# Kernel optimization log

Hardware: AMD Instinct MI355X
Metric: run time of the kernel (lower is better)

Reference implementation:

```python
import jax, jax.numpy as jnp
import numpy as np

D_MODEL = 1024
NUM_HEADS = 16
DEPTH = D_MODEL // NUM_HEADS


def setup_inputs() -> dict:
    key = jax.random.key(0)
    ks = jax.random.split(key, 6)
    B, S = 2, 2048
    scale = 1.0 / np.sqrt(D_MODEL)
    return {
        "q": jax.random.normal(ks[0], (B, S, D_MODEL), jnp.float32),
        "k": jax.random.normal(ks[1], (B, S, D_MODEL), jnp.float32),
        "v": jax.random.normal(ks[2], (B, S, D_MODEL), jnp.float32),
        "wq": jax.random.normal(ks[3], (D_MODEL, D_MODEL), jnp.float32) * scale,
        "wk": jax.random.normal(ks[4], (D_MODEL, D_MODEL), jnp.float32) * scale,
        "wv": jax.random.normal(ks[5], (D_MODEL, D_MODEL), jnp.float32) * scale,
    }


def reference(q, k, v, wq, wk, wv):
    B, S, _ = q.shape
    # Linear projections (nn.Linear: x @ W.T), then split heads -> [B,H,S,depth]
    def split(x):
        return x.reshape(B, -1, NUM_HEADS, DEPTH).transpose(0, 2, 1, 3)
    Q = split(q @ wq.T)
    K = split(k @ wk.T)
    V = split(v @ wv.T)
    scores = jnp.einsum("bhqd,bhkd->bhqk", Q, K) / np.sqrt(DEPTH).astype(np.float32)
    attn = jax.nn.softmax(scores, axis=-1)
    out = jnp.einsum("bhqk,bhkd->bhqd", attn, V)
    # merge heads; note: original forward never applies self.dense
    return out.transpose(0, 2, 1, 3).reshape(B, S, D_MODEL)
```

## Files before the change

### kernel.cpp

```cpp
#include <hip/hip_runtime.h>
#include <hip/hip_bf16.h>
#include <stdint.h>

#define B_SZ 2
#define S_LEN 2048
#define DM 1024
#define NH 16
#define DEPTH 64
#define M_ROWS (B_SZ * S_LEN)
#define SCALE_Q 0.1803368801111144f

typedef __attribute__((ext_vector_type(8))) short bf16x8;
typedef __attribute__((ext_vector_type(4))) float f32x4;
typedef __attribute__((ext_vector_type(16))) float f32x16;

__device__ __forceinline__ unsigned short f2bf(float x) {
    union { float f; unsigned u; } a; a.f = x;
    unsigned r = a.u + 0x7FFF + ((a.u >> 16) & 1);
    return (unsigned short)(r >> 16);
}

__device__ __forceinline__ void async_ld16(const unsigned short* g, void* l) {
    __builtin_amdgcn_global_load_lds(
        (const __attribute__((address_space(1))) void*)g,
        (__attribute__((address_space(3))) void*)l,
        16, 0, 0);
}


__global__ __launch_bounds__(256)
void convert_kernel(const float* __restrict__ q, const float* __restrict__ k,
                    const float* __restrict__ v, const float* __restrict__ wq,
                    const float* __restrict__ wk, const float* __restrict__ wv,
                    unsigned short* __restrict__ dst) {
    const int z = blockIdx.y;
    const float* src = (z == 0) ? q : (z == 1) ? k : (z == 2) ? v
                     : (z == 3) ? wq : (z == 4) ? wk : wv;
    const size_t n4  = (z < 3) ? ((size_t)M_ROWS * DM / 4) : ((size_t)DM * DM / 4);
    const size_t off = (z < 3) ? ((size_t)z * M_ROWS * DM)
                               : ((size_t)3 * M_ROWS * DM + (size_t)(z - 3) * DM * DM);
    unsigned short* d = dst + off;
    const size_t stride = (size_t)gridDim.x * blockDim.x;
    for (size_t i = (size_t)blockIdx.x * blockDim.x + threadIdx.x; i < n4; i += stride) {
        float4 x = ((const float4*)src)[i];
        ushort4 p;
        p.x = f2bf(x.x); p.y = f2bf(x.y); p.z = f2bf(x.z); p.w = f2bf(x.w);
        ((ushort4*)d)[i] = p;
    }
}

__global__ __launch_bounds__(256)
void proj_gemm3_kernel(const unsigned short* __restrict__ Xall,
                       const unsigned short* __restrict__ Wall,
                       unsigned short* __restrict__ Call) {
    __shared__ unsigned short As[128 * 64];
    __shared__ unsigned short Bs[128 * 64];

    const int z = blockIdx.z;
    const unsigned short* X = Xall + (size_t)z * M_ROWS * DM;
    const unsigned short* W = Wall + (size_t)z * DM * DM;
    unsigned short* C = Call + (size_t)z * M_ROWS * DM;

    const int tid  = threadIdx.x;
    const int wave = tid >> 6;
    const int lane = tid & 63;
    const int l32  = lane & 31;
    const int s    = lane >> 5;
    const int m0 = blockIdx.x * 128;
    const int n0 = blockIdx.y * 128;
    const int wm = (wave >> 1) * 64;
    const int wn = (wave & 1) * 64;

    const int r8 = lane >> 3;
    const int sc = (lane & 7) ^ r8;

    f32x16 acc[2][2];
#pragma unroll
    for (int mi = 0; mi < 2; ++mi)
#pragma unroll
        for (int ni = 0; ni < 2; ++ni)
#pragma unroll
            for (int r = 0; r < 16; ++r) acc[mi][ni][r] = 0.f;

    for (int k0 = 0; k0 < DM; k0 += 64) {
#pragma unroll
        for (int i = 0; i < 4; ++i) {
            const int r = i * 32 + wave * 8 + r8;
            async_ld16(X + (size_t)(m0 + r) * DM + k0 + sc * 8,
                       (char*)As + i * 4096 + wave * 1024);
            async_ld16(W + (size_t)(n0 + r) * DM + k0 + sc * 8,
                       (char*)Bs + i * 4096 + wave * 1024);
        }
        __syncthreads();

#pragma unroll
        for (int ch = 0; ch < 4; ++ch) {
            bf16x8 af[2], bfr[2];
#pragma unroll
            for (int mi = 0; mi < 2; ++mi) {
                const int row = wm + mi * 32 + l32;
                af[mi] = *(const bf16x8*)&As[row * 64 + (((2 * ch + s) ^ (row & 7)) * 8)];
            }
#pragma unroll
            for (int ni = 0; ni < 2; ++ni) {
                const int row = wn + ni * 32 + l32;
                bfr[ni] = *(const bf16x8*)&Bs[row * 64 + (((2 * ch + s) ^ (row & 7)) * 8)];
            }
#pragma unroll
            for (int mi = 0; mi < 2; ++mi)
#pragma unroll
                for (int ni = 0; ni < 2; ++ni)
                    acc[mi][ni] = __builtin_amdgcn_mfma_f32_32x32x16_bf16(
                        af[mi], bfr[ni], acc[mi][ni], 0, 0, 0);
        }
        __syncthreads();
    }

    const float scale = (z == 0) ? SCALE_Q : 1.0f;
#pragma unroll
    for (int mi = 0; mi < 2; ++mi)
#pragma unroll
        for (int ni = 0; ni < 2; ++ni)
#pragma unroll
            for (int r = 0; r < 16; ++r) {
                const int row = m0 + wm + mi * 32 + (r & 3) + 8 * (r >> 2) + 4 * s;
                const int col = n0 + wn + ni * 32 + l32;
                C[(size_t)row * DM + col] = f2bf(acc[mi][ni][r] * scale);
            }
}

__global__ __launch_bounds__(256)
void vtrans_kernel(const unsigned short* __restrict__ Vp,
                   unsigned short* __restrict__ Vt) {
    __shared__ unsigned short Ls[64 * 72];
    const int tr = blockIdx.x;
    const int h  = blockIdx.y;
    const int tid = threadIdx.x;

#pragma unroll
    for (int i = 0; i < 2; ++i) {
        const int id = i * 256 + tid;
        const int r = id >> 3, c = id & 7;
        bf16x8 v8 = *(const bf16x8*)&Vp[(size_t)(tr * 64 + r) * DM + h * 64 + c * 8];
        *(bf16x8*)&Ls[r * 72 + ((c ^ (r & 7)) * 8)] = v8;
    }
    __syncthreads();

    const int b = tr >> 5;
    const int col0 = (tr & 31) * 64;
#pragma unroll
    for (int i = 0; i < 2; ++i) {
        const int id = i * 256 + tid;
        const int d = id >> 3, c2 = id & 7;
        unsigned short tmp[8];
#pragma unroll
        for (int j = 0; j < 8; ++j) {
            const int t = c2 * 8 + j;
            tmp[j] = Ls[t * 72 + (((d >> 3) ^ (t & 7)) * 8) + (d & 7)];
        }
        *(bf16x8*)&Vt[(size_t)((b * NH + h) * DEPTH + d) * S_LEN + col0 + c2 * 8] =
            *(const bf16x8*)tmp;
    }
}

__global__ __launch_bounds__(64)
void attn4_kernel(const unsigned short* __restrict__ Qp,
                  const unsigned short* __restrict__ Kp,
                  const unsigned short* __restrict__ Vt,
                  float* __restrict__ out) {
    __shared__ __align__(16) char smem[40960];
    unsigned short* Ks = (unsigned short*)smem;
    unsigned short* Vs = (unsigned short*)(smem + 16384);
    unsigned short* Ps = (unsigned short*)(smem + 32768);

    const int lane = threadIdx.x & 63;
    const int l32  = lane & 31;
    const int s    = lane >> 5;
    const int q0 = blockIdx.x * 64;
    const int h  = blockIdx.y;
    const int b  = blockIdx.z;

    const int r8 = lane >> 3;
    const int sc = (lane & 7) ^ r8;

    const unsigned short* Kg = Kp + (size_t)(b * S_LEN) * DM + h * DEPTH;
    const unsigned short* Vg = Vt + (size_t)((b * NH + h) * DEPTH) * S_LEN;

    bf16x8 qf[2][4];
#pragma unroll
    for (int nq = 0; nq < 2; ++nq) {
        const unsigned short* p =
            Qp + (size_t)(b * S_LEN + q0 + nq * 32 + l32) * DM + h * DEPTH;
#pragma unroll
        for (int ch = 0; ch < 4; ++ch)
            qf[nq][ch] = *(const bf16x8*)(p + ch * 16 + s * 8);
    }

    f32x16 oacc[2][2];
    float lacc[2] = {0.f, 0.f};
#pragma unroll
    for (int db = 0; db < 2; ++db)
#pragma unroll
        for (int nq = 0; nq < 2; ++nq)
#pragma unroll
            for (int r = 0; r < 16; ++r) oacc[db][nq][r] = 0.f;

#pragma unroll
    for (int i = 0; i < 8; ++i) {
        async_ld16(Kg + (size_t)(i * 8 + r8) * DM + sc * 8, (char*)Ks + i * 1024);
        async_ld16(Vg + (size_t)(i * 8 + r8) * S_LEN + sc * 8, (char*)Vs + i * 1024);
    }

    for (int it = 0; it < S_LEN / 64; ++it) {
        const int buf = it & 1;
        if (it < S_LEN / 64 - 1) {
            const int t1 = (it + 1) * 64;
            char* kd = (char*)Ks + (buf ^ 1) * 8192;
            char* vd = (char*)Vs + (buf ^ 1) * 8192;
#pragma unroll
            for (int i = 0; i < 8; ++i) {
                async_ld16(Kg + (size_t)(t1 + i * 8 + r8) * DM + sc * 8,
                           kd + i * 1024);
                async_ld16(Vg + (size_t)(i * 8 + r8) * S_LEN + t1 + sc * 8,
                           vd + i * 1024);
            }
            __builtin_amdgcn_s_waitcnt(0x4F70);
        } else {
            __builtin_amdgcn_s_waitcnt(0x0F70);
        }
        __builtin_amdgcn_sched_barrier(0);

        const unsigned short* Kb = Ks + buf * 4096;
        const unsigned short* Vb = Vs + buf * 4096;

#pragma unroll
        for (int tb = 0; tb < 2; ++tb) {
            f32x16 s0, s1;
#pragma unroll
            for (int r = 0; r < 16; ++r) { s0[r] = 0.f; s1[r] = 0.f; }
            const int trow = tb * 32 + l32;
#pragma unroll
            for (int ch = 0; ch < 4; ++ch) {
                bf16x8 kf = *(const bf16x8*)
                    &Kb[trow * 64 + (((2 * ch + s) ^ (trow & 7)) * 8)];
                s0 = __builtin_amdgcn_mfma_f32_32x32x16_bf16(kf, qf[0][ch], s0, 0, 0, 0);
                s1 = __builtin_amdgcn_mfma_f32_32x32x16_bf16(kf, qf[1][ch], s1, 0, 0, 0);
            }
#pragma unroll
            for (int nq = 0; nq < 2; ++nq) {
                const int qq = nq * 32 + l32;
#pragma unroll
                for (int a = 0; a < 4; ++a) {
                    union { float f; unsigned u; } e0, e1, e2, e3;
                    e0.f = __builtin_amdgcn_exp2f(nq ? s1[4 * a + 0] : s0[4 * a + 0]);
                    e1.f = __builtin_amdgcn_exp2f(nq ? s1[4 * a + 1] : s0[4 * a + 1]);
                    e2.f = __builtin_amdgcn_exp2f(nq ? s1[4 * a + 2] : s0[4 * a + 2]);
                    e3.f = __builtin_amdgcn_exp2f(nq ? s1[4 * a + 3] : s0[4 * a + 3]);
                    union { unsigned u; float f; } t0, t1, t2, t3;
                    t0.u = e0.u & 0xFFFF0000u; t1.u = e1.u & 0xFFFF0000u;
                    t2.u = e2.u & 0xFFFF0000u; t3.u = e3.u & 0xFFFF0000u;
                    lacc[nq] += (t0.f + t1.f) + (t2.f + t3.f);
                    const int slot = (4 * tb + a) ^ (qq & 7);
                    *(unsigned*)&Ps[qq * 64 + slot * 8 + 4 * s] =
                        (e0.u >> 16) | (e1.u & 0xFFFF0000u);
                    *(unsigned*)&Ps[qq * 64 + slot * 8 + 4 * s + 2] =
                        (e2.u >> 16) | (e3.u & 0xFFFF0000u);
                }
            }
        }
        __builtin_amdgcn_sched_barrier(0);

#pragma unroll
        for (int ch = 0; ch < 4; ++ch) {
            bf16x8 pf0 = *(const bf16x8*)
                &Ps[l32 * 64 + (((2 * ch + s) ^ (l32 & 7)) * 8)];
            bf16x8 pf1 = *(const bf16x8*)
                &Ps[(32 + l32) * 64 + (((2 * ch + s) ^ (l32 & 7)) * 8)];
#pragma unroll
            for (int db = 0; db < 2; ++db) {
                const int drow = db * 32 + l32;
                bf16x8 vf = *(const bf16x8*)
                    &Vb[drow * 64 + (((2 * ch + s) ^ (drow & 7)) * 8)];
                oacc[db][0] = __builtin_amdgcn_mfma_f32_32x32x16_bf16(
                    vf, pf0, oacc[db][0], 0, 0, 0);
                oacc[db][1] = __builtin_amdgcn_mfma_f32_32x32x16_bf16(
                    vf, pf1, oacc[db][1], 0, 0, 0);
            }
        }
        __builtin_amdgcn_sched_barrier(0);
    }

    const float l0 = lacc[0] + __shfl_xor(lacc[0], 32, 64);
    const float l1 = lacc[1] + __shfl_xor(lacc[1], 32, 64);
    const float inv0 = 1.0f / l0, inv1 = 1.0f / l1;

    __builtin_amdgcn_s_waitcnt(0xC07F);
    __builtin_amdgcn_sched_barrier(0);
    float* Of = (float*)(smem + 16384);
#pragma unroll
    for (int db = 0; db < 2; ++db)
#pragma unroll
        for (int nq = 0; nq < 2; ++nq) {
            const int qq = nq * 32 + l32;
            const float inv = nq ? inv1 : inv0;
#pragma unroll
            for (int r = 0; r < 16; ++r) {
                const int d = db * 32 + (r & 3) + 8 * (r >> 2) + 4 * s;
                Of[qq * 68 + d] = oacc[db][nq][r] * inv;
            }
        }
    __builtin_amdgcn_sched_barrier(0);
#pragma unroll
    for (int i = 0; i < 16; ++i) {
        const int row = i * 4 + (lane >> 4);
        const int c4 = lane & 15;
        float4 v = *(const float4*)&Of[row * 68 + c4 * 4];
        *(float4*)&out[(size_t)(b * S_LEN + q0 + row) * DM + h * DEPTH + c4 * 4] = v;
    }
}

#define LDK 72

__global__ __launch_bounds__(256)
void proj_gemm_kernel(const float* __restrict__ q, const float* __restrict__ k,
                      const float* __restrict__ v, const float* __restrict__ wq,
                      const float* __restrict__ wk, const float* __restrict__ wv,
                      unsigned short* __restrict__ Qp, unsigned short* __restrict__ Kp,
                      unsigned short* __restrict__ Vp) {
    __shared__ unsigned short As[128 * LDK];
    __shared__ unsigned short Bs[128 * LDK];

    const int z = blockIdx.z;
    const float* __restrict__ X = (z == 0) ? q : (z == 1) ? k : v;
    const float* __restrict__ W = (z == 0) ? wq : (z == 1) ? wk : wv;
    unsigned short* __restrict__ C = (z == 0) ? Qp : (z == 1) ? Kp : Vp;

    const int tid  = threadIdx.x;
    const int wave = tid >> 6;
    const int lane = tid & 63;
    const int quad = lane >> 4;
    const int l16  = lane & 15;
    const int m0 = blockIdx.x * 128;
    const int n0 = blockIdx.y * 128;
    const int wm = (wave >> 1) * 64;
    const int wn = (wave & 1) * 64;

    f32x4 acc[4][4];
#pragma unroll
    for (int mt = 0; mt < 4; ++mt)
#pragma unroll
        for (int nt = 0; nt < 4; ++nt)
            acc[mt][nt] = (f32x4){0.f, 0.f, 0.f, 0.f};

    for (int k0 = 0; k0 < DM; k0 += 64) {
#pragma unroll
        for (int vv = 0; vv < 8; ++vv) {
            int vecid = tid + 256 * vv;
            int r  = vecid >> 4;
            int c4 = vecid & 15;
            const float4 xa = *(const float4*)&X[(size_t)(m0 + r) * DM + k0 + c4 * 4];
            ushort4 pa;
            pa.x = f2bf(xa.x); pa.y = f2bf(xa.y); pa.z = f2bf(xa.z); pa.w = f2bf(xa.w);
            *(ushort4*)&As[r * LDK + c4 * 4] = pa;
            const float4 xb = *(const float4*)&W[(size_t)(n0 + r) * DM + k0 + c4 * 4];
            ushort4 pb;
            pb.x = f2bf(xb.x); pb.y = f2bf(xb.y); pb.z = f2bf(xb.z); pb.w = f2bf(xb.w);
            *(ushort4*)&Bs[r * LDK + c4 * 4] = pb;
        }
        __syncthreads();

#pragma unroll
        for (int kc = 0; kc < 2; ++kc) {
            bf16x8 af[4], bfr[4];
#pragma unroll
            for (int mt = 0; mt < 4; ++mt)
                af[mt] = *(const bf16x8*)&As[(wm + mt * 16 + l16) * LDK + kc * 32 + quad * 8];
#pragma unroll
            for (int nt = 0; nt < 4; ++nt)
                bfr[nt] = *(const bf16x8*)&Bs[(wn + nt * 16 + l16) * LDK + kc * 32 + quad * 8];
#pragma unroll
            for (int mt = 0; mt < 4; ++mt)
#pragma unroll
                for (int nt = 0; nt < 4; ++nt)
                    acc[mt][nt] = __builtin_amdgcn_mfma_f32_16x16x32_bf16(
                        af[mt], bfr[nt], acc[mt][nt], 0, 0, 0);
        }
        __syncthreads();
    }

#pragma unroll
    for (int mt = 0; mt < 4; ++mt)
#pragma unroll
        for (int nt = 0; nt < 4; ++nt)
#pragma unroll
            for (int r = 0; r < 4; ++r) {
                int row = m0 + wm + mt * 16 + quad * 4 + r;
                int col = n0 + wn + nt * 16 + l16;
                C[(size_t)row * DM + col] = f2bf(acc[mt][nt][r]);
            }
}

__global__ __launch_bounds__(256)
void attn_kernel(const unsigned short* __restrict__ Qp,
                 const unsigned short* __restrict__ Kp,
                 const unsigned short* __restrict__ Vp,
                 float* __restrict__ out) {
    __shared__ unsigned short Ks[64 * LDK];
    __shared__ unsigned short Vtl[64 * LDK];
    __shared__ unsigned short Ps[4 * 16 * LDK];

    const int tid  = threadIdx.x;
    const int wave = tid >> 6;
    const int lane = tid & 63;
    const int quad = lane >> 4;
    const int l16  = lane & 15;
    const int q0 = blockIdx.x * 64;
    const int h  = blockIdx.y;
    const int b  = blockIdx.z;
    const int wbase = wave * 16 * LDK;

    bf16x8 qf[2];
    {
        size_t row = (size_t)b * S_LEN + q0 + wave * 16 + l16;
        const unsigned short* p = Qp + row * DM + h * DEPTH;
        qf[0] = *(const bf16x8*)(p + quad * 8);
        qf[1] = *(const bf16x8*)(p + 32 + quad * 8);
    }

    float m_i[4], l_i[4];
    f32x4 accO[4];
#pragma unroll
    for (int r = 0; r < 4; ++r) { m_i[r] = -1e30f; l_i[r] = 0.f; }
#pragma unroll
    for (int f = 0; f < 4; ++f) accO[f] = (f32x4){0.f, 0.f, 0.f, 0.f};

    for (int t0 = 0; t0 < S_LEN; t0 += 64) {
#pragma unroll
        for (int vv = 0; vv < 2; ++vv) {
            int vecid = tid + 256 * vv;
            int r  = vecid >> 3;
            int cv = vecid & 7;
            size_t grow = (size_t)(b * S_LEN + t0 + r) * DM + h * DEPTH + cv * 8;
            *(bf16x8*)&Ks[r * LDK + cv * 8] = *(const bf16x8*)(Kp + grow);
            bf16x8 vvv = *(const bf16x8*)(Vp + grow);
#pragma unroll
            for (int j = 0; j < 8; ++j)
                Vtl[(cv * 8 + j) * LDK + r] = ((const unsigned short*)&vvv)[j];
        }
        __syncthreads();

        f32x4 sc4[4];
#pragma unroll
        for (int nt = 0; nt < 4; ++nt) {
            f32x4 a = (f32x4){0.f, 0.f, 0.f, 0.f};
            bf16x8 kf0 = *(const bf16x8*)&Ks[(nt * 16 + l16) * LDK + quad * 8];
            bf16x8 kf1 = *(const bf16x8*)&Ks[(nt * 16 + l16) * LDK + 32 + quad * 8];
            a = __builtin_amdgcn_mfma_f32_16x16x32_bf16(qf[0], kf0, a, 0, 0, 0);
            a = __builtin_amdgcn_mfma_f32_16x16x32_bf16(qf[1], kf1, a, 0, 0, 0);
            sc4[nt] = a;
        }
#pragma unroll
        for (int nt = 0; nt < 4; ++nt)
#pragma unroll
            for (int r = 0; r < 4; ++r) sc4[nt][r] *= 0.125f;

#pragma unroll
        for (int r = 0; r < 4; ++r) {
            float mx = fmaxf(fmaxf(sc4[0][r], sc4[1][r]), fmaxf(sc4[2][r], sc4[3][r]));
#pragma unroll
            for (int off = 1; off < 16; off <<= 1)
                mx = fmaxf(mx, __shfl_xor(mx, off, 64));
            float mnew = fmaxf(m_i[r], mx);
            float alpha = __expf(m_i[r] - mnew);
            float rs = 0.f;
#pragma unroll
            for (int nt = 0; nt < 4; ++nt) {
                float p = __expf(sc4[nt][r] - mnew);
                sc4[nt][r] = p;
                rs += p;
            }
#pragma unroll
            for (int off = 1; off < 16; off <<= 1)
                rs += __shfl_xor(rs, off, 64);
            l_i[r] = l_i[r] * alpha + rs;
            m_i[r] = mnew;
#pragma unroll
            for (int f = 0; f < 4; ++f) accO[f][r] *= alpha;
        }

#pragma unroll
        for (int nt = 0; nt < 4; ++nt)
#pragma unroll
            for (int r = 0; r < 4; ++r)
                Ps[wbase + (quad * 4 + r) * LDK + nt * 16 + l16] = f2bf(sc4[nt][r]);
        __syncthreads();

        bf16x8 pf0 = *(const bf16x8*)&Ps[wbase + l16 * LDK + quad * 8];
        bf16x8 pf1 = *(const bf16x8*)&Ps[wbase + l16 * LDK + 32 + quad * 8];
#pragma unroll
        for (int f = 0; f < 4; ++f) {
            bf16x8 vf0 = *(const bf16x8*)&Vtl[(f * 16 + l16) * LDK + quad * 8];
            bf16x8 vf1 = *(const bf16x8*)&Vtl[(f * 16 + l16) * LDK + 32 + quad * 8];
            accO[f] = __builtin_amdgcn_mfma_f32_16x16x32_bf16(pf0, vf0, accO[f], 0, 0, 0);
            accO[f] = __builtin_amdgcn_mfma_f32_16x16x32_bf16(pf1, vf1, accO[f], 0, 0, 0);
        }
        __syncthreads();
    }

#pragma unroll
    for (int f = 0; f < 4; ++f)
#pragma unroll
        for (int r = 0; r < 4; ++r) {
            size_t row = (size_t)b * S_LEN + q0 + wave * 16 + quad * 4 + r;
            out[row * DM + h * DEPTH + f * 16 + l16] = accO[f][r] / l_i[r];
        }
}

extern "C" void kernel_launch(void* const* d_in, const int* in_sizes, int n_in,
                              void* d_out, int out_size, void* d_ws, size_t ws_size,
                              hipStream_t stream) {
    const float* q  = (const float*)d_in[0];
    const float* k  = (const float*)d_in[1];
    const float* v  = (const float*)d_in[2];
    const float* wq = (const float*)d_in[3];
    const float* wk = (const float*)d_in[4];
    const float* wv = (const float*)d_in[5];
    float* out = (float*)d_out;

    unsigned short* ws = (unsigned short*)d_ws;
    const size_t NPROJ = (size_t)M_ROWS * DM;
    const size_t NW    = (size_t)DM * DM;

    const size_t need = (3 * NPROJ + 3 * NW + 3 * NPROJ) * sizeof(unsigned short);

    if (ws_size >= need) {
        unsigned short* Xbf = ws;
        unsigned short* Wbf = ws + 3 * NPROJ;
        unsigned short* Cp  = ws + 3 * NPROJ + 3 * NW;
        unsigned short* Qp  = Cp;
        unsigned short* Kp  = Cp + NPROJ;
        unsigned short* Vp  = Cp + 2 * NPROJ;
        unsigned short* Vt  = ws;

        convert_kernel<<<dim3(256, 6), 256, 0, stream>>>(q, k, v, wq, wk, wv, Xbf);
        proj_gemm3_kernel<<<dim3(M_ROWS / 128, DM / 128, 3), 256, 0, stream>>>(Xbf, Wbf, Cp);
        vtrans_kernel<<<dim3(M_ROWS / 64, NH), 256, 0, stream>>>(Vp, Vt);
        attn4_kernel<<<dim3(S_LEN / 64, NH, B_SZ), 64, 0, stream>>>(Qp, Kp, Vt, out);
    } else {
        unsigned short* Qp = ws;
        unsigned short* Kp = ws + NPROJ;
        unsigned short* Vp = ws + 2 * NPROJ;
        proj_gemm_kernel<<<dim3(M_ROWS / 128, DM / 128, 3), 256, 0, stream>>>(
            q, k, v, wq, wk, wv, Qp, Kp, Vp);
        attn_kernel<<<dim3(S_LEN / 64, NH, B_SZ), 256, 0, stream>>>(Qp, Kp, Vp, out);
    }
}
```

Measured before the change: 213.5 us.

## Split attention over key halves with two-wave blocks and a combine pass

Replaces the one-wave attention kernel with two-wave blocks that share K/V tiles in LDS and split the key sequence into two halves across the grid. Each half writes unnormalized partial outputs and row sums, and a new combine kernel adds them and normalizes. K is now staged in 32-row tiles and V in 64-column tiles, with a block barrier each iteration. The aim is more parallelism and better reuse of K/V loads across waves. The cost is extra global traffic for the partial outputs, an extra kernel launch, and per-iteration synchronization.

```diff
diff --git a/kernel.cpp b/kernel.cpp
--- a/kernel.cpp
+++ b/kernel.cpp
@@ -18,6 +18,10 @@
     union { float f; unsigned u; } a; a.f = x;
     unsigned r = a.u + 0x7FFF + ((a.u >> 16) & 1);
     return (unsigned short)(r >> 16);
+}
+
+__device__ __forceinline__ bf16x8 u4_to_bf8(uint4 u) {
+    union { uint4 a; bf16x8 b; } c; c.a = u; return c.b;
 }
 
 __device__ __forceinline__ void async_ld16(const unsigned short* g, void* l) {
@@ -163,28 +167,38 @@
     }
 }
 
-__global__ __launch_bounds__(64)
-void attn4_kernel(const unsigned short* __restrict__ Qp,
+__global__ __launch_bounds__(128, 2)
+void attn8_kernel(const unsigned short* __restrict__ Qp,
                   const unsigned short* __restrict__ Kp,
                   const unsigned short* __restrict__ Vt,
-                  float* __restrict__ out) {
-    __shared__ __align__(16) char smem[40960];
+                  float* __restrict__ out,
+                  float* __restrict__ Op1,
+                  float* __restrict__ lp) {
+    __shared__ __align__(16) char smem[34816];
     unsigned short* Ks = (unsigned short*)smem;
-    unsigned short* Vs = (unsigned short*)(smem + 16384);
-    unsigned short* Ps = (unsigned short*)(smem + 32768);
-
-    const int lane = threadIdx.x & 63;
+    unsigned short* Vs = (unsigned short*)(smem + 8192);
+    unsigned int*   Ps = (unsigned int*)(smem + 24576);
+
+    const int tid  = threadIdx.x;
+    const int w    = tid >> 6;
+    const int lane = tid & 63;
     const int l32  = lane & 31;
     const int s    = lane >> 5;
-    const int q0 = blockIdx.x * 64;
+    const int r8   = lane >> 3;
+    const int sc   = (lane & 7) ^ r8;
+
+    const int q0 = blockIdx.x * 128 + w * 64;
     const int h  = blockIdx.y;
-    const int b  = blockIdx.z;
-
-    const int r8 = lane >> 3;
-    const int sc = (lane & 7) ^ r8;
-
-    const unsigned short* Kg = Kp + (size_t)(b * S_LEN) * DM + h * DEPTH;
-    const unsigned short* Vg = Vt + (size_t)((b * NH + h) * DEPTH) * S_LEN;
+    const int z  = blockIdx.z;
+    const int b     = z >> 1;
+    const int split = z & 1;
+    const int tbase = split * 1024;
+
+    const unsigned short* Kg = Kp + (size_t)(b * S_LEN + tbase) * DM + h * DEPTH;
+    const unsigned short* Vg = Vt + (size_t)((b * NH + h) * DEPTH) * S_LEN + tbase;
+    float* obase = split ? Op1 : out;
+    float* lbase = lp + (size_t)split * M_ROWS * NH;
+    unsigned int* PsW = Ps + w * 1280;
 
     bf16x8 qf[2][4];
 #pragma unroll
@@ -206,117 +220,155 @@
             for (int r = 0; r < 16; ++r) oacc[db][nq][r] = 0.f;
 
 #pragma unroll
-    for (int i = 0; i < 8; ++i) {
-        async_ld16(Kg + (size_t)(i * 8 + r8) * DM + sc * 8, (char*)Ks + i * 1024);
-        async_ld16(Vg + (size_t)(i * 8 + r8) * S_LEN + sc * 8, (char*)Vs + i * 1024);
-    }
-
-    for (int it = 0; it < S_LEN / 64; ++it) {
-        const int buf = it & 1;
-        if (it < S_LEN / 64 - 1) {
-            const int t1 = (it + 1) * 64;
-            char* kd = (char*)Ks + (buf ^ 1) * 8192;
-            char* vd = (char*)Vs + (buf ^ 1) * 8192;
-#pragma unroll
-            for (int i = 0; i < 8; ++i) {
-                async_ld16(Kg + (size_t)(t1 + i * 8 + r8) * DM + sc * 8,
+    for (int i = 0; i < 2; ++i)
+        async_ld16(Kg + (size_t)(w * 16 + i * 8 + r8) * DM + sc * 8,
+                   (char*)Ks + w * 2048 + i * 1024);
+#pragma unroll
+    for (int i = 0; i < 4; ++i)
+        async_ld16(Vg + (size_t)(w * 32 + i * 8 + r8) * S_LEN + sc * 8,
+                   (char*)Vs + w * 4096 + i * 1024);
+
+    for (int it = 0; it < 32; ++it) {
+        const int kb = it & 1;
+        const int vb = (it >> 1) & 1;
+
+        __syncthreads();
+
+        if (it < 31) {
+            const int tk = (it + 1) * 32;
+            char* kd = (char*)Ks + (kb ^ 1) * 4096 + w * 2048;
+#pragma unroll
+            for (int i = 0; i < 2; ++i)
+                async_ld16(Kg + (size_t)(tk + w * 16 + i * 8 + r8) * DM + sc * 8,
                            kd + i * 1024);
-                async_ld16(Vg + (size_t)(i * 8 + r8) * S_LEN + t1 + sc * 8,
+        }
+        if (!(it & 1) && it < 30) {
+            const int tv = ((it >> 1) + 1) * 64;
+            char* vd = (char*)Vs + (vb ^ 1) * 8192 + w * 4096;
+#pragma unroll
+            for (int i = 0; i < 4; ++i)
+                async_ld16(Vg + (size_t)(w * 32 + i * 8 + r8) * S_LEN + tv + sc * 8,
                            vd + i * 1024);
-            }
-            __builtin_amdgcn_s_waitcnt(0x4F70);
-        } else {
-            __builtin_amdgcn_s_waitcnt(0x0F70);
-        }
-        __builtin_amdgcn_sched_barrier(0);
-
-        const unsigned short* Kb = Ks + buf * 4096;
-        const unsigned short* Vb = Vs + buf * 4096;
-
-#pragma unroll
-        for (int tb = 0; tb < 2; ++tb) {
-            f32x16 s0, s1;
-#pragma unroll
-            for (int r = 0; r < 16; ++r) { s0[r] = 0.f; s1[r] = 0.f; }
-            const int trow = tb * 32 + l32;
-#pragma unroll
-            for (int ch = 0; ch < 4; ++ch) {
-                bf16x8 kf = *(const bf16x8*)
-                    &Kb[trow * 64 + (((2 * ch + s) ^ (trow & 7)) * 8)];
-                s0 = __builtin_amdgcn_mfma_f32_32x32x16_bf16(kf, qf[0][ch], s0, 0, 0, 0);
-                s1 = __builtin_amdgcn_mfma_f32_32x32x16_bf16(kf, qf[1][ch], s1, 0, 0, 0);
-            }
+        }
+
+        const unsigned short* Kb = Ks + kb * 2048;
+        const unsigned short* Vb = Vs + vb * 4096;
+        const int vcb = (it & 1) * 4;
+
+        f32x16 s0, s1;
+#pragma unroll
+        for (int r = 0; r < 16; ++r) { s0[r] = 0.f; s1[r] = 0.f; }
+#pragma unroll
+        for (int ch = 0; ch < 4; ++ch) {
+            bf16x8 kf = *(const bf16x8*)
+                &Kb[l32 * 64 + (((2 * ch + s) ^ (l32 & 7)) * 8)];
+            s0 = __builtin_amdgcn_mfma_f32_32x32x16_bf16(kf, qf[0][ch], s0, 0, 0, 0);
+            s1 = __builtin_amdgcn_mfma_f32_32x32x16_bf16(kf, qf[1][ch], s1, 0, 0, 0);
+        }
+
+#pragma unroll
+        for (int nq = 0; nq < 2; ++nq) {
+            const int qq = nq * 32 + l32;
+            const int xq = (qq ^ (qq >> 2)) & 3;
+#pragma unroll
+            for (int a = 0; a < 4; ++a) {
+                union { float f; unsigned u; } e0, e1, e2, e3;
+                e0.f = __builtin_amdgcn_exp2f(nq ? s1[4 * a + 0] : s0[4 * a + 0]);
+                e1.f = __builtin_amdgcn_exp2f(nq ? s1[4 * a + 1] : s0[4 * a + 1]);
+                e2.f = __builtin_amdgcn_exp2f(nq ? s1[4 * a + 2] : s0[4 * a + 2]);
+                e3.f = __builtin_amdgcn_exp2f(nq ? s1[4 * a + 3] : s0[4 * a + 3]);
+                union { unsigned u; float f; } t0, t1, t2, t3;
+                t0.u = e0.u & 0xFFFF0000u; t1.u = e1.u & 0xFFFF0000u;
+                t2.u = e2.u & 0xFFFF0000u; t3.u = e3.u & 0xFFFF0000u;
+                lacc[nq] += (t0.f + t1.f) + (t2.f + t3.f);
+                uint2 pk;
+                pk.x = (e0.u >> 16) | (e1.u & 0xFFFF0000u);
+                pk.y = (e2.u >> 16) | (e3.u & 0xFFFF0000u);
+                *(uint2*)&PsW[qq * 20 + ((a ^ xq) * 4) + 2 * s] = pk;
+            }
+        }
+
+        asm volatile("" ::: "memory");
+
+#pragma unroll
+        for (int ch = 0; ch < 2; ++ch) {
+            bf16x8 pf[2];
 #pragma unroll
             for (int nq = 0; nq < 2; ++nq) {
                 const int qq = nq * 32 + l32;
-#pragma unroll
-                for (int a = 0; a < 4; ++a) {
-                    union { float f; unsigned u; } e0, e1, e2, e3;
-                    e0.f = __builtin_amdgcn_exp2f(nq ? s1[4 * a + 0] : s0[4 * a + 0]);
-                    e1.f = __builtin_amdgcn_exp2f(nq ? s1[4 * a + 1] : s0[4 * a + 1]);
-                    e2.f = __builtin_amdgcn_exp2f(nq ? s1[4 * a + 2] : s0[4 * a + 2]);
-                    e3.f = __builtin_amdgcn_exp2f(nq ? s1[4 * a + 3] : s0[4 * a + 3]);
-                    union { unsigned u; float f; } t0, t1, t2, t3;
-                    t0.u = e0.u & 0xFFFF0000u; t1.u = e1.u & 0xFFFF0000u;
-                    t2.u = e2.u & 0xFFFF0000u; t3.u = e3.u & 0xFFFF0000u;
-                    lacc[nq] += (t0.f + t1.f) + (t2.f + t3.f);
-                    const int slot = (4 * tb + a) ^ (qq & 7);
-                    *(unsigned*)&Ps[qq * 64 + slot * 8 + 4 * s] =
-                        (e0.u >> 16) | (e1.u & 0xFFFF0000u);
-                    *(unsigned*)&Ps[qq * 64 + slot * 8 + 4 * s + 2] =
-                        (e2.u >> 16) | (e3.u & 0xFFFF0000u);
-                }
-            }
-        }
-        __builtin_amdgcn_sched_barrier(0);
-
-#pragma unroll
-        for (int ch = 0; ch < 4; ++ch) {
-            bf16x8 pf0 = *(const bf16x8*)
-                &Ps[l32 * 64 + (((2 * ch + s) ^ (l32 & 7)) * 8)];
-            bf16x8 pf1 = *(const bf16x8*)
-                &Ps[(32 + l32) * 64 + (((2 * ch + s) ^ (l32 & 7)) * 8)];
+                const int slot = (2 * ch + s) ^ ((qq ^ (qq >> 2)) & 3);
+                uint4 pu = *(const uint4*)&PsW[qq * 20 + slot * 4];
+                pf[nq] = u4_to_bf8(pu);
+            }
 #pragma unroll
             for (int db = 0; db < 2; ++db) {
                 const int drow = db * 32 + l32;
                 bf16x8 vf = *(const bf16x8*)
-                    &Vb[drow * 64 + (((2 * ch + s) ^ (drow & 7)) * 8)];
+                    &Vb[drow * 64 + (((vcb + 2 * ch + s) ^ (drow & 7)) * 8)];
                 oacc[db][0] = __builtin_amdgcn_mfma_f32_32x32x16_bf16(
-                    vf, pf0, oacc[db][0], 0, 0, 0);
+                    vf, pf[0], oacc[db][0], 0, 0, 0);
                 oacc[db][1] = __builtin_amdgcn_mfma_f32_32x32x16_bf16(
-                    vf, pf1, oacc[db][1], 0, 0, 0);
-            }
-        }
-        __builtin_amdgcn_sched_barrier(0);
+                    vf, pf[1], oacc[db][1], 0, 0, 0);
+            }
+        }
+        asm volatile("" ::: "memory");
     }
 
     const float l0 = lacc[0] + __shfl_xor(lacc[0], 32, 64);
     const float l1 = lacc[1] + __shfl_xor(lacc[1], 32, 64);
-    const float inv0 = 1.0f / l0, inv1 = 1.0f / l1;
-
-    __builtin_amdgcn_s_waitcnt(0xC07F);
-    __builtin_amdgcn_sched_barrier(0);
-    float* Of = (float*)(smem + 16384);
-#pragma unroll
-    for (int db = 0; db < 2; ++db)
-#pragma unroll
-        for (int nq = 0; nq < 2; ++nq) {
-            const int qq = nq * 32 + l32;
-            const float inv = nq ? inv1 : inv0;
-#pragma unroll
-            for (int r = 0; r < 16; ++r) {
-                const int d = db * 32 + (r & 3) + 8 * (r >> 2) + 4 * s;
-                Of[qq * 68 + d] = oacc[db][nq][r] * inv;
-            }
-        }
-    __builtin_amdgcn_sched_barrier(0);
-#pragma unroll
-    for (int i = 0; i < 16; ++i) {
-        const int row = i * 4 + (lane >> 4);
-        const int c4 = lane & 15;
-        float4 v = *(const float4*)&Of[row * 68 + c4 * 4];
-        *(float4*)&out[(size_t)(b * S_LEN + q0 + row) * DM + h * DEPTH + c4 * 4] = v;
-    }
+    if (s == 0) {
+        lbase[(size_t)(b * S_LEN + q0 + l32) * NH + h]      = l0;
+        lbase[(size_t)(b * S_LEN + q0 + 32 + l32) * NH + h] = l1;
+    }
+
+    asm volatile("" ::: "memory");
+    float* Of = (float*)PsW;
+#pragma unroll
+    for (int c = 0; c < 4; ++c) {
+        const int nq = c >> 1;
+        if ((l32 >> 4) == (c & 1)) {
+            const int qh = l32 & 15;
+#pragma unroll
+            for (int db = 0; db < 2; ++db)
+#pragma unroll
+                for (int m = 0; m < 4; ++m) {
+                    float4 v;
+                    v.x = oacc[db][nq][4 * m + 0];
+                    v.y = oacc[db][nq][4 * m + 1];
+                    v.z = oacc[db][nq][4 * m + 2];
+                    v.w = oacc[db][nq][4 * m + 3];
+                    *(float4*)&Of[qh * 68 + db * 32 + 8 * m + 4 * s] = v;
+                }
+        }
+        asm volatile("" ::: "memory");
+#pragma unroll
+        for (int i = 0; i < 4; ++i) {
+            const int row = i * 4 + (lane >> 4);
+            const int c4 = lane & 15;
+            float4 v = *(const float4*)&Of[row * 68 + c4 * 4];
+            *(float4*)&obase[(size_t)(b * S_LEN + q0 + c * 16 + row) * DM
+                             + h * DEPTH + c4 * 4] = v;
+        }
+        asm volatile("" ::: "memory");
+    }
+}
+
+__global__ __launch_bounds__(256)
+void combine_kernel(float* __restrict__ out, const float* __restrict__ Op1,
+                    const float* __restrict__ lp) {
+    const int i4 = blockIdx.x * 256 + threadIdx.x;
+    const int row = i4 >> 8;
+    const int c4  = i4 & 255;
+    const int h   = c4 >> 4;
+    const float l = lp[row * NH + h] + lp[M_ROWS * NH + row * NH + h];
+    const float inv = 1.0f / l;
+    float4 a = ((const float4*)out)[i4];
+    float4 bq = ((const float4*)Op1)[i4];
+    a.x = (a.x + bq.x) * inv;
+    a.y = (a.y + bq.y) * inv;
+    a.z = (a.z + bq.z) * inv;
+    a.w = (a.w + bq.w) * inv;
+    ((float4*)out)[i4] = a;
 }
 
 #define LDK 72
@@ -541,11 +593,15 @@
         unsigned short* Kp  = Cp + NPROJ;
         unsigned short* Vp  = Cp + 2 * NPROJ;
         unsigned short* Vt  = ws;
+        float*          Op1 = (float*)(ws + NPROJ);
+        float*          lp  = (float*)(ws + 3 * NPROJ);
 
         convert_kernel<<<dim3(256, 6), 256, 0, stream>>>(q, k, v, wq, wk, wv, Xbf);
         proj_gemm3_kernel<<<dim3(M_ROWS / 128, DM / 128, 3), 256, 0, stream>>>(Xbf, Wbf, Cp);
         vtrans_kernel<<<dim3(M_ROWS / 64, NH), 256, 0, stream>>>(Vp, Vt);
-        attn4_kernel<<<dim3(S_LEN / 64, NH, B_SZ), 64, 0, stream>>>(Qp, Kp, Vt, out);
+        attn8_kernel<<<dim3(S_LEN / 128, NH, 4), 128, 0, stream>>>(
+            Qp, Kp, Vt, out, Op1, lp);
+        combine_kernel<<<dim3(M_ROWS * DM / 4 / 256), 256, 0, stream>>>(out, Op1, lp);
     } else {
         unsigned short* Qp = ws;
         unsigned short* Kp = ws + NPROJ;
```

Result: faster. 198.8 us (-6.9%).
